# Kernel optimization log

Hardware: AMD Instinct MI355X
Metric: run time of the kernel (lower is better)

The kernel has to match this reference:

```python
import jax, jax.numpy as jnp
import numpy as np

B, L, D, H = 4, 1024, 1024, 16
HD = D // H


def setup_inputs() -> dict:
    key = jax.random.key(0)
    ks = jax.random.split(key, 64)
    it = iter(ks)

    def w(shape, s=0.02):
        return jax.random.normal(next(it), shape, dtype=jnp.float32) * s

    inp = {
        'seq_features': jax.random.normal(next(it), (B, L, D), dtype=jnp.float32),
        'struct_features': jax.random.normal(next(it), (B, L, D), dtype=jnp.float32),
        'attention_mask': jnp.ones((B, L), dtype=bool),
    }
    for p in ('s2s', 't2s'):
        inp[f'{p}_qw'] = w((D, D)); inp[f'{p}_qb'] = w((D,))
        inp[f'{p}_kw'] = w((D, D)); inp[f'{p}_kb'] = w((D,))
        inp[f'{p}_vw'] = w((D, D)); inp[f'{p}_vb'] = w((D,))
        inp[f'{p}_ow'] = w((D, D)); inp[f'{p}_ob'] = w((D,))
        inp[f'{p}_g'] = jnp.ones((D,), dtype=jnp.float32)
        inp[f'{p}_beta'] = jnp.zeros((D,), dtype=jnp.float32)
        inp[f'{p}_temp'] = jnp.ones((1,), dtype=jnp.float32)
    inp['fus_w1'] = w((2 * D, D)); inp['fus_b1'] = w((D,))
    inp['fus_w2'] = w((D, D)); inp['fus_b2'] = w((D,))
    return inp


def _layernorm(x, g, b, eps=1e-5):
    m = x.mean(-1, keepdims=True)
    v = ((x - m) ** 2).mean(-1, keepdims=True)
    return (x - m) / jnp.sqrt(v + eps) * g + b


def _cross_attn(q_in, kv_in, mask, qw, qb, kw, kb, vw, vb, ow, ob, g, beta, temp):
    # q_in, kv_in: (B, L, D); mask: (B, L) bool
    Q = (q_in @ qw + qb).reshape(B, L, H, HD).transpose(0, 2, 1, 3)
    K = (kv_in @ kw + kb).reshape(B, L, H, HD).transpose(0, 2, 1, 3)
    V = (kv_in @ vw + vb).reshape(B, L, H, HD).transpose(0, 2, 1, 3)
    scores = jnp.einsum('bhqd,bhkd->bhqk', Q, K) / np.float32(np.sqrt(HD))
    scores = scores / jnp.maximum(temp, 0.1)
    scores = jnp.where(mask[:, None, None, :], scores, -jnp.inf)
    aw = jax.nn.softmax(scores, axis=-1)  # dropout is identity in eval mode
    ctx = jnp.einsum('bhqk,bhkd->bhqd', aw, V).transpose(0, 2, 1, 3).reshape(B, L, D)
    out = _layernorm(ctx @ ow + ob + q_in, g, beta)
    return out, aw.mean(axis=1)


def _fusion(x, w1, b1, w2, b2):
    return jax.nn.gelu(x @ w1 + b1, approximate=False) @ w2 + b2


def reference(seq_features, struct_features, attention_mask,
              s2s_qw, s2s_qb, s2s_kw, s2s_kb, s2s_vw, s2s_vb, s2s_ow, s2s_ob, s2s_g, s2s_beta, s2s_temp,
              t2s_qw, t2s_qb, t2s_kw, t2s_kb, t2s_vw, t2s_vb, t2s_ow, t2s_ob, t2s_g, t2s_beta, t2s_temp,
              fus_w1, fus_b1, fus_w2, fus_b2):
    seq_upd, s2s_attn = _cross_attn(seq_features, struct_features, attention_mask,
                                    s2s_qw, s2s_qb, s2s_kw, s2s_kb, s2s_vw, s2s_vb,
                                    s2s_ow, s2s_ob, s2s_g, s2s_beta, s2s_temp)
    struct_upd, t2s_attn = _cross_attn(struct_features, seq_features, attention_mask,
                                       t2s_qw, t2s_qb, t2s_kw, t2s_kb, t2s_vw, t2s_vb,
                                       t2s_ow, t2s_ob, t2s_g, t2s_beta, t2s_temp)
    seq_fused = _fusion(jnp.concatenate([seq_upd, seq_features], axis=-1), fus_w1, fus_b1, fus_w2, fus_b2)
    struct_fused = _fusion(jnp.concatenate([struct_upd, struct_features], axis=-1), fus_w1, fus_b1, fus_w2, fus_b2)
    return seq_fused, struct_fused, s2s_attn, t2s_attn
```

## Files before the change

### kernel.cpp

```cpp
#include <hip/hip_runtime.h>
#include <hip/hip_bf16.h>
#include <stdint.h>
#include <stddef.h>

#define LL 1024
#define DD 1024

typedef __attribute__((ext_vector_type(8))) unsigned short ushort8;
typedef __attribute__((ext_vector_type(8))) __bf16 bf16x8;
typedef __attribute__((ext_vector_type(4))) __bf16 bf16x4;
typedef __attribute__((ext_vector_type(4))) float f32x4;
typedef __attribute__((ext_vector_type(4))) short short4v;
typedef unsigned short u16;

static __device__ __forceinline__ float b2f(u16 u) {
    union { uint32_t i; float f; } x; x.i = ((uint32_t)u) << 16; return x.f;
}
static __device__ __forceinline__ u16 f2b(float f) {
    union { float f; uint32_t i; } x; x.f = f;
    uint32_t r = (x.i + 0x7fffu + ((x.i >> 16) & 1u)) >> 16;
    return (u16)r;
}

#define GL16(gsrc, ldst)                                                      \
    __builtin_amdgcn_global_load_lds(                                         \
        (const __attribute__((address_space(1))) void*)(gsrc),                \
        (__attribute__((address_space(3))) void*)(ldst), 16, 0, 0)

struct WPtrs { const float* p[10]; };

__launch_bounds__(256)
__global__ void wcvt2_k(WPtrs wp, u16* __restrict__ dst)
{
    __shared__ float ls[64][65];
    const int bx = blockIdx.x;
    const float* src; size_t dbase; int n0, k0, Kd;
    if (bx < 2048) {
        const int mat = bx >> 8, t = bx & 255;
        n0 = (t >> 4) * 64; k0 = (t & 15) * 64;
        src = wp.p[mat]; dbase = (size_t)mat << 20; Kd = 1024;
    } else if (bx < 2560) {
        const int t = bx - 2048;
        n0 = (t >> 5) * 64; k0 = (t & 31) * 64;
        src = wp.p[8]; dbase = (size_t)8 << 20; Kd = 2048;
    } else {
        const int t = bx - 2560;
        n0 = (t >> 4) * 64; k0 = (t & 15) * 64;
        src = wp.p[9]; dbase = (size_t)10 << 20; Kd = 1024;
    }
    const int tid = threadIdx.x;
    const int rr = tid >> 2, cc0 = (tid & 3) * 16;
#pragma unroll
    for (int i = 0; i < 4; i++) {
        const f32x4 v = *(const f32x4*)(src + (size_t)(k0 + rr) * 1024 + n0 + cc0 + i * 4);
        *(f32x4*)&ls[rr][cc0 + i * 4] = v;
    }
    __syncthreads();
    const int nn = tid >> 2, ks0 = (tid & 3) * 16;
    u16* dp = dst + dbase + (size_t)(n0 + nn) * Kd + k0 + ks0;
#pragma unroll
    for (int i = 0; i < 4; i++) {
        short4v o;
#pragma unroll
        for (int j = 0; j < 4; j++) o[j] = (short)f2b(ls[ks0 + i * 4 + j][nn]);
        *(short4v*)(dp + i * 4) = o;
    }
}

__launch_bounds__(256)
__global__ void cvt_in_k(const float* __restrict__ a, const float* __restrict__ b,
                         u16* __restrict__ oa, u16* __restrict__ ob)
{
    const size_t i = ((size_t)blockIdx.x * 256 + threadIdx.x) * 8;
    f32x4 v0 = *(const f32x4*)(a + i), v1 = *(const f32x4*)(a + i + 4);
    f32x4 w0 = *(const f32x4*)(b + i), w1 = *(const f32x4*)(b + i + 4);
    ushort8 ra, rb;
#pragma unroll
    for (int j = 0; j < 4; j++) {
        ra[j] = f2b(v0[j]); ra[j + 4] = f2b(v1[j]);
        rb[j] = f2b(w0[j]); rb[j + 4] = f2b(w1[j]);
    }
    *(ushort8*)&oa[i] = ra;
    *(ushort8*)&ob[i] = rb;
}

__device__ __forceinline__ void gemm_core(
    const u16* __restrict__ A1, const u16* __restrict__ A2,
    const u16* __restrict__ WT, int K, int arow, int n0, int tid,
    u16* As, u16* Bt, f32x4 acc[4][4])
{
    const int lane = tid & 63, wid = tid >> 6;
    const int wr = wid >> 1, wc = wid & 1;
    const int fr = lane & 15, fq = lane >> 4;
    const int srow8 = lane >> 3, sslot = lane & 7;
    const int scol = ((sslot ^ srow8) * 8);
#pragma unroll
    for (int i = 0; i < 4; i++)
#pragma unroll
        for (int j = 0; j < 4; j++) acc[i][j] = f32x4{0.f, 0.f, 0.f, 0.f};

    auto stage = [&](int buf, int k0s) {
        const u16* Asrc = A1; int kc = k0s;
        if (A2 != nullptr && k0s >= 1024) { Asrc = A2; kc = k0s - 1024; }
#pragma unroll
        for (int p = 0; p < 4; p++) {
            const int row = p * 32 + wid * 8 + srow8;
            GL16(Asrc + (size_t)(arow + row) * 1024 + kc + scol,
                 As + buf * 8192 + (p * 32 + wid * 8) * 64);
            GL16(WT + (size_t)(n0 + row) * K + k0s + scol,
                 Bt + buf * 8192 + (p * 32 + wid * 8) * 64);
        }
    };

    stage(0, 0);
    __syncthreads();
    int cur = 0;
    for (int k0 = 0; k0 < K; k0 += 64) {
        if (k0 + 64 < K) stage(cur ^ 1, k0 + 64);
        const u16* Asb = As + cur * 8192;
        const u16* Btb = Bt + cur * 8192;
#pragma unroll
        for (int kk = 0; kk < 2; kk++) {
            const int rs = ((kk * 4 + fq) ^ (fr & 7)) * 8;
            bf16x8 af[4], bfv[4];
#pragma unroll
            for (int mi = 0; mi < 4; mi++)
                af[mi] = *(const bf16x8*)&Asb[(wr * 64 + mi * 16 + fr) * 64 + rs];
#pragma unroll
            for (int ni = 0; ni < 4; ni++)
                bfv[ni] = *(const bf16x8*)&Btb[(wc * 64 + ni * 16 + fr) * 64 + rs];
#pragma unroll
            for (int mi = 0; mi < 4; mi++)
#pragma unroll
                for (int ni = 0; ni < 4; ni++)
                    acc[mi][ni] = __builtin_amdgcn_mfma_f32_16x16x32_bf16(
                        af[mi], bfv[ni], acc[mi][ni], 0, 0, 0);
        }
        __syncthreads();
        cur ^= 1;
    }
}

struct ProjArgs {
    const u16* Au[2];
    const u16* wtQ[2]; const u16* wtK[2]; const u16* wtV[2];
    const float* bQ[2]; const float* bK[2]; const float* bV[2];
    const float* temp[2];
    u16* outQ[2]; u16* outK[2]; u16* outV[2];
};

__launch_bounds__(256)
__global__ void proj2_k(ProjArgs a)
{
    __shared__ __align__(16) u16 As[2 * 128 * 64];
    __shared__ __align__(16) u16 Bt[2 * 128 * 64];
    const int id = blockIdx.x;
    const int nid = (id & 7) * 192 + (id >> 3);
    const int pass = (nid >= 768);
    const int nid2 = nid - pass * 768;
    const int nt = nid2 % 24, mt = nid2 / 24;
    const int seg = nt >> 3, nc = (nt & 7) * 128, m0 = mt * 128;
    const u16* Au = a.Au[pass];
    const u16* WT = (seg == 0) ? a.wtQ[pass] : ((seg == 1) ? a.wtK[pass] : a.wtV[pass]);
    const float* bias = (seg == 0) ? a.bQ[pass] : ((seg == 1) ? a.bK[pass] : a.bV[pass]);
    u16* outQ = a.outQ[pass]; u16* outK = a.outK[pass]; u16* outV = a.outV[pass];
    const int tid = threadIdx.x, lane = tid & 63, wid = tid >> 6;
    const int wr = wid >> 1, wc = wid & 1, fr = lane & 15, fq = lane >> 4;
    const float qs = 1.44269504f * 0.125f / fmaxf(a.temp[pass][0], 0.1f);

    f32x4 acc[4][4];
    gemm_core(Au, nullptr, WT, 1024, m0, nc, tid, As, Bt, acc);

#pragma unroll
    for (int mi = 0; mi < 4; mi++) {
#pragma unroll
        for (int ni = 0; ni < 4; ni++) {
            const int col = nc + wc * 64 + ni * 16 + fr;
            const float bv = bias[col];
#pragma unroll
            for (int r = 0; r < 4; r++) {
                const int row = m0 + wr * 64 + mi * 16 + fq * 4 + r;
                const float v = acc[mi][ni][r] + bv;
                if (seg == 0) {
                    outQ[(size_t)row * 1024 + col] = f2b(v * qs);
                } else if (seg == 1) {
                    const int b2 = row >> 10, kk = row & 1023;
                    const int h2 = col >> 6, dd2 = col & 63;
                    const int kt = kk >> 4, fr2 = kk & 15;
                    const int plane = dd2 >> 5, fq2 = (dd2 >> 3) & 3, j = dd2 & 7;
                    outK[(size_t)(b2 * 16 + h2) * 65536 + kt * 1024 + plane * 512
                         + (fq2 * 16 + fr2) * 8 + j] = f2b(v);
                } else {
                    const int b2 = row >> 10, kk = row & 1023;
                    const int h2 = col >> 6, dd2 = col & 63;
                    outV[(size_t)(b2 * 16 + h2) * 65536 + (kk >> 4) * 1024
                         + (dd2 >> 4) * 256 + ((kk >> 2) & 3) * 64
                         + (dd2 & 15) * 4 + (kk & 3)] = f2b(v);
                }
            }
        }
    }
}

template <int EPI>
__launch_bounds__(256)
__global__ void mgemm_k(const u16* __restrict__ A1a, const u16* __restrict__ A1b,
                        const u16* __restrict__ A2a, const u16* __restrict__ A2b,
                        const u16* __restrict__ WTa, const u16* __restrict__ WTb,
                        const float* __restrict__ ba, const float* __restrict__ bb,
                        const float* __restrict__ ra, const float* __restrict__ rb,
                        void* __restrict__ oa_, void* __restrict__ ob_, int K)
{
    __shared__ __align__(16) u16 As[2 * 128 * 64];
    __shared__ __align__(16) u16 Bt[2 * 128 * 64];
    const int id = blockIdx.x;
    const int nid = (id & 7) * 64 + (id >> 3);
    const int n0 = (nid & 7) * 128, m0g = (nid >> 3) * 128;
    const int half = (m0g >= 4096), arow = m0g & 4095;
    const u16* A1 = half ? A1b : A1a;
    const u16* A2 = half ? A2b : A2a;
    const u16* WT = half ? WTb : WTa;
    const float* bias = half ? bb : ba;
    const float* res = half ? rb : ra;
    void* outp = half ? ob_ : oa_;
    const int tid = threadIdx.x, lane = tid & 63, wid = tid >> 6;
    const int wr = wid >> 1, wc = wid & 1, fr = lane & 15, fq = lane >> 4;

    f32x4 acc[4][4];
    gemm_core(A1, A2, WT, K, arow, n0, tid, As, Bt, acc);

#pragma unroll
    for (int mi = 0; mi < 4; mi++) {
#pragma unroll
        for (int ni = 0; ni < 4; ni++) {
            const int col = n0 + wc * 64 + ni * 16 + fr;
            const float bv = bias[col];
#pragma unroll
            for (int r = 0; r < 4; r++) {
                const int row = arow + wr * 64 + mi * 16 + fq * 4 + r;
                float v = acc[mi][ni][r] + bv;
                if (EPI == 1) {
                    v = 0.5f * v * (1.0f + erff(v * 0.70710678118f));
                    ((u16*)outp)[(size_t)row * 1024 + col] = f2b(v);
                } else if (EPI == 2) {
                    v += res[(size_t)row * 1024 + col];
                    ((float*)outp)[(size_t)row * 1024 + col] = v;
                } else {
                    ((float*)outp)[(size_t)row * 1024 + col] = v;
                }
            }
        }
    }
}

struct AttnArgs {
    const u16* Q[2]; const u16* KT[2]; const u16* Vt[2];
    u16* ctx[2]; float* iarr;
};

__global__ __launch_bounds__(512, 2)
void attnS3_k(AttnArgs a)
{
    const int id = blockIdx.x;
    const int b = id & 3, pass = (id >> 2) & 1, hg = (id >> 3) & 1;
    const int q0 = (id >> 4) * 64;
    const int tid = threadIdx.x, lane = tid & 63, wid = tid >> 6;
    const int fr = lane & 15, fq = lane >> 4;
    const int head = hg * 8 + wid;

    const u16* Q = a.Q[pass];
    bf16x8 bq0[4], bq1[4];
#pragma unroll
    for (int s = 0; s < 4; s++) {
        const u16* qp = Q + ((size_t)(b * LL + q0 + s * 16 + fr)) * DD + head * 64 + fq * 8;
        bq0[s] = *(const bf16x8*)(qp);
        bq1[s] = *(const bf16x8*)(qp + 32);
    }
    const u16* ktb = a.KT[pass] + (size_t)(b * 16 + head) * 65536 + lane * 8;
    const u16* vtb = a.Vt[pass] + (size_t)(b * 16 + head) * 65536 + lane * 4;

    float l[4] = {0.f, 0.f, 0.f, 0.f};
    f32x4 oa[4][4];
#pragma unroll
    for (int s = 0; s < 4; s++)
#pragma unroll
        for (int j = 0; j < 4; j++) oa[s][j] = f32x4{0.f, 0.f, 0.f, 0.f};

    for (int kt = 0; kt < 64; kt++) {
        const bf16x8 ka0 = *(const bf16x8*)(ktb + kt * 1024);
        const bf16x8 ka1 = *(const bf16x8*)(ktb + kt * 1024 + 512);
        short4v ps[4];
#pragma unroll
        for (int s = 0; s < 4; s++) {
            f32x4 c{0.f, 0.f, 0.f, 0.f};
            c = __builtin_amdgcn_mfma_f32_16x16x32_bf16(ka0, bq0[s], c, 0, 0, 0);
            c = __builtin_amdgcn_mfma_f32_16x16x32_bf16(ka1, bq1[s], c, 0, 0, 0);
            const float p0 = exp2f(c[0]), p1 = exp2f(c[1]);
            const float p2 = exp2f(c[2]), p3 = exp2f(c[3]);
            l[s] += (p0 + p1) + (p2 + p3);
            bf16x4 pb;
            pb[0] = (__bf16)p0; pb[1] = (__bf16)p1;
            pb[2] = (__bf16)p2; pb[3] = (__bf16)p3;
            ps[s] = __builtin_bit_cast(short4v, pb);
        }
        const u16* vp = vtb + (size_t)kt * 1024;
        const short4v va0 = *(const short4v*)(vp);
        const short4v va1 = *(const short4v*)(vp + 256);
        const short4v va2 = *(const short4v*)(vp + 512);
        const short4v va3 = *(const short4v*)(vp + 768);
#pragma unroll
        for (int s = 0; s < 4; s++) {
            oa[s][0] = __builtin_amdgcn_mfma_f32_16x16x16bf16_1k(va0, ps[s], oa[s][0], 0, 0, 0);
            oa[s][1] = __builtin_amdgcn_mfma_f32_16x16x16bf16_1k(va1, ps[s], oa[s][1], 0, 0, 0);
            oa[s][2] = __builtin_amdgcn_mfma_f32_16x16x16bf16_1k(va2, ps[s], oa[s][2], 0, 0, 0);
            oa[s][3] = __builtin_amdgcn_mfma_f32_16x16x16bf16_1k(va3, ps[s], oa[s][3], 0, 0, 0);
        }
    }
#pragma unroll
    for (int s = 0; s < 4; s++) {
        l[s] += __shfl_xor(l[s], 16);
        l[s] += __shfl_xor(l[s], 32);
        const float inv = 1.f / l[s];
        if (fq == 0) {
            const int qg = b * LL + q0 + s * 16 + fr;
            a.iarr[((pass * 16 + head) << 12) + qg] = inv;
        }
        u16* cp = a.ctx[pass] + ((size_t)(b * LL + q0 + s * 16 + fr)) * DD + head * 64 + fq * 4;
#pragma unroll
        for (int r = 0; r < 4; r++) {
            cp[r]      = f2b(oa[s][0][r] * inv);
            cp[16 + r] = f2b(oa[s][1][r] * inv);
            cp[32 + r] = f2b(oa[s][2][r] * inv);
            cp[48 + r] = f2b(oa[s][3][r] * inv);
        }
    }
}

__global__ __launch_bounds__(512, 2)
void meanM3_k(const u16* __restrict__ Q0, const u16* __restrict__ Q1,
              const u16* __restrict__ KT0, const u16* __restrict__ KT1,
              const float* __restrict__ iarr,
              float* __restrict__ d0, float* __restrict__ d1a,
              float* __restrict__ d1b)
{
    const int id = blockIdx.x;
    const int b = id & 3, pass = (id >> 2) & 1, kh = (id >> 3) & 1;
    const int q0 = (id >> 4) * 64;
    const int tid = threadIdx.x, lane = tid & 63, wid = tid >> 6;
    const int fr = lane & 15, fq = lane >> 4;
    const u16* Q = pass ? Q1 : Q0;
    const u16* KT = pass ? KT1 : KT0;
    __shared__ float il[16][64];
#pragma unroll
    for (int i = 0; i < 2; i++) {
        const int idx = tid + i * 512;
        const int h = idx >> 6, qq = idx & 63;
        il[h][qq] = iarr[((pass * 16 + h) << 12) + b * LL + q0 + qq];
    }
    __syncthreads();

    const int ktbase = kh * 32 + wid * 4;
    f32x4 msacc[4][4];
#pragma unroll
    for (int s = 0; s < 4; s++)
#pragma unroll
        for (int i = 0; i < 4; i++) msacc[s][i] = f32x4{0.f, 0.f, 0.f, 0.f};
    for (int h = 0; h < 16; h++) {
        bf16x8 cq0[4], cq1[4];
        float ih[4];
#pragma unroll
        for (int s = 0; s < 4; s++) {
            const u16* qp = Q + ((size_t)(b * LL + q0 + s * 16 + fr)) * DD + h * 64 + fq * 8;
            cq0[s] = *(const bf16x8*)(qp);
            cq1[s] = *(const bf16x8*)(qp + 32);
            ih[s] = il[h][s * 16 + fr];
        }
        const u16* kb = KT + (size_t)(b * 16 + h) * 65536 + lane * 8;
#pragma unroll
        for (int ktl = 0; ktl < 4; ktl++) {
            const int kt = ktbase + ktl;
            const bf16x8 ka0 = *(const bf16x8*)(kb + kt * 1024);
            const bf16x8 ka1 = *(const bf16x8*)(kb + kt * 1024 + 512);
#pragma unroll
            for (int s = 0; s < 4; s++) {
                f32x4 c{0.f, 0.f, 0.f, 0.f};
                c = __builtin_amdgcn_mfma_f32_16x16x32_bf16(ka0, cq0[s], c, 0, 0, 0);
                c = __builtin_amdgcn_mfma_f32_16x16x32_bf16(ka1, cq1[s], c, 0, 0, 0);
#pragma unroll
                for (int r = 0; r < 4; r++)
                    msacc[s][ktl][r] += exp2f(c[r]) * ih[s];
            }
        }
    }
#pragma unroll
    for (int s = 0; s < 4; s++) {
        float* dst; size_t rowbase;
        const int row = q0 + s * 16 + fr;
        if (pass == 0) {
            dst = d0; rowbase = (size_t)(b * LL + row) * 1024;
        } else {
            dst = (b < 2) ? d1a : d1b;
            rowbase = (size_t)((b & 1) * LL + row) * 1024;
        }
#pragma unroll
        for (int ktl = 0; ktl < 4; ktl++) {
            const f32x4 v = msacc[s][ktl] * (1.f / 16.f);
            *(f32x4*)&dst[rowbase + (ktbase + ktl) * 16 + fq * 4] = v;
        }
    }
}

__launch_bounds__(256)
__global__ void ln2_k(const float* __restrict__ y0, const float* __restrict__ y1,
                      const float* __restrict__ g0, const float* __restrict__ g1,
                      const float* __restrict__ be0, const float* __restrict__ be1,
                      u16* __restrict__ o0, u16* __restrict__ o1)
{
    const int rg = blockIdx.x, tid = threadIdx.x, lane = tid & 63, wid = tid >> 6;
    const int half = rg >> 12, rl = rg & 4095;
    const float* yp = (half ? y1 : y0) + (size_t)rl * 1024;
    const float* g = half ? g1 : g0;
    const float* be = half ? be1 : be0;
    u16* op = (half ? o1 : o0) + (size_t)rl * 1024;
    __shared__ float rsum[4], rsq[4];
    f32x4 v = *(const f32x4*)(yp + tid * 4);
    float s = v[0] + v[1] + v[2] + v[3];
    float sq = v[0]*v[0] + v[1]*v[1] + v[2]*v[2] + v[3]*v[3];
    for (int off = 1; off < 64; off <<= 1) {
        s  += __shfl_xor(s,  off, 64);
        sq += __shfl_xor(sq, off, 64);
    }
    if (lane == 0) { rsum[wid] = s; rsq[wid] = sq; }
    __syncthreads();
    const float S  = rsum[0] + rsum[1] + rsum[2] + rsum[3];
    const float SQ = rsq[0] + rsq[1] + rsq[2] + rsq[3];
    const float mean = S * (1.f / 1024.f);
    const float var  = SQ * (1.f / 1024.f) - mean * mean;
    const float rstd = rsqrtf(var + 1e-5f);
#pragma unroll
    for (int j = 0; j < 4; j++) {
        const int i = tid * 4 + j;
        op[i] = f2b((v[j] - mean) * rstd * g[i] + be[i]);
    }
}

extern "C" void kernel_launch(void* const* d_in, const int* in_sizes, int n_in,
                              void* d_out, int out_size, void* d_ws, size_t ws_size,
                              hipStream_t stream)
{
    (void)in_sizes; (void)n_in; (void)out_size; (void)ws_size;
    const float* seq = (const float*)d_in[0];
    const float* str = (const float*)d_in[1];
    const float* s2s_qb = (const float*)d_in[4];
    const float* s2s_kb = (const float*)d_in[6];
    const float* s2s_vb = (const float*)d_in[8];
    const float* s2s_ob = (const float*)d_in[10];
    const float* s2s_g  = (const float*)d_in[11];
    const float* s2s_be = (const float*)d_in[12];
    const float* s2s_t  = (const float*)d_in[13];
    const float* t2s_qb = (const float*)d_in[15];
    const float* t2s_kb = (const float*)d_in[17];
    const float* t2s_vb = (const float*)d_in[19];
    const float* t2s_ob = (const float*)d_in[21];
    const float* t2s_g  = (const float*)d_in[22];
    const float* t2s_be = (const float*)d_in[23];
    const float* t2s_t  = (const float*)d_in[24];
    const float* fb1 = (const float*)d_in[26];
    const float* fb2 = (const float*)d_in[28];

    char* ws = (char*)d_ws;
    u16*   Qs2s = (u16*)(ws);
    u16*   Ks2s = (u16*)(ws + ((size_t)8  << 20));
    u16*   Vs2s = (u16*)(ws + ((size_t)16 << 20));
    u16*   Qt2s = (u16*)(ws + ((size_t)24 << 20));
    u16*   Kt2s = (u16*)(ws + ((size_t)32 << 20));
    u16*   Vt2s = (u16*)(ws + ((size_t)40 << 20));
    float* mean1a = (float*)(ws + ((size_t)16 << 20));
    float* mean1b = (float*)(ws + ((size_t)40 << 20));
    float* y0   = (float*)(ws);
    float* y1   = (float*)(ws + ((size_t)24 << 20));
    u16*   sup  = (u16*)(ws + ((size_t)16 << 20));
    u16*   tup  = (u16*)(ws + ((size_t)40 << 20));
    u16*   sequ2 = (u16*)(ws);
    u16*   stru2 = (u16*)(ws + ((size_t)8 << 20));
    u16*   hid  = (u16*)(ws + ((size_t)24 << 20));
    u16*   fw2T = (u16*)(ws);

    float* out = (float*)d_out;
    const size_t M4 = (size_t)4 * 1024 * 1024;
    u16* wb = (u16*)d_out;
    u16* sequ = (u16*)((char*)d_out + ((size_t)32 << 20));
    u16* stru = (u16*)((char*)d_out + ((size_t)40 << 20));
    float* iarr = (float*)((char*)d_out + ((size_t)22 << 20));
    u16* ctx0 = (u16*)(out + 3 * M4);
    u16* ctx1 = ctx0 + (size_t)4096 * 1024;

    WPtrs wp;
    wp.p[0] = (const float*)d_in[3];
    wp.p[1] = (const float*)d_in[5];
    wp.p[2] = (const float*)d_in[7];
    wp.p[3] = (const float*)d_in[9];
    wp.p[4] = (const float*)d_in[14];
    wp.p[5] = (const float*)d_in[16];
    wp.p[6] = (const float*)d_in[18];
    wp.p[7] = (const float*)d_in[20];
    wp.p[8] = (const float*)d_in[25];
    wp.p[9] = (const float*)d_in[27];
    wcvt2_k<<<2816, 256, 0, stream>>>(wp, wb);
    cvt_in_k<<<2048, 256, 0, stream>>>(seq, str, sequ, stru);

    const dim3 gb(256);

    ProjArgs pa;
    pa.Au[0] = sequ;                         pa.Au[1] = stru;
    pa.wtQ[0] = wb;                          pa.wtQ[1] = wb + ((size_t)4 << 20);
    pa.wtK[0] = wb + ((size_t)5 << 20);      pa.wtK[1] = wb + ((size_t)1 << 20);
    pa.wtV[0] = wb + ((size_t)6 << 20);      pa.wtV[1] = wb + ((size_t)2 << 20);
    pa.bQ[0] = s2s_qb;  pa.bQ[1] = t2s_qb;
    pa.bK[0] = t2s_kb;  pa.bK[1] = s2s_kb;
    pa.bV[0] = t2s_vb;  pa.bV[1] = s2s_vb;
    pa.temp[0] = s2s_t; pa.temp[1] = t2s_t;
    pa.outQ[0] = Qs2s;  pa.outQ[1] = Qt2s;
    pa.outK[0] = Kt2s;  pa.outK[1] = Ks2s;
    pa.outV[0] = Vt2s;  pa.outV[1] = Vs2s;
    proj2_k<<<1536, gb, 0, stream>>>(pa);

    AttnArgs aa;
    aa.Q[0] = Qs2s;  aa.Q[1] = Qt2s;
    aa.KT[0] = Ks2s; aa.KT[1] = Kt2s;
    aa.Vt[0] = Vs2s; aa.Vt[1] = Vt2s;
    aa.ctx[0] = ctx0; aa.ctx[1] = ctx1;
    aa.iarr = iarr;
    attnS3_k<<<256, 512, 0, stream>>>(aa);

    meanM3_k<<<256, 512, 0, stream>>>(Qs2s, Qt2s, Ks2s, Kt2s, iarr,
                                      out + 2 * M4, mean1a, mean1b);

    mgemm_k<2><<<512, gb, 0, stream>>>(
        ctx0, ctx1, nullptr, nullptr,
        wb + ((size_t)3 << 20), wb + ((size_t)7 << 20),
        s2s_ob, t2s_ob, seq, str, y0, y1, 1024);

    hipMemcpyAsync(out + 3 * M4, mean1a, (size_t)8 << 20,
                   hipMemcpyDeviceToDevice, stream);
    hipMemcpyAsync((char*)(out + 3 * M4) + ((size_t)8 << 20), mean1b,
                   (size_t)8 << 20, hipMemcpyDeviceToDevice, stream);

    ln2_k<<<8192, gb, 0, stream>>>(y0, y1, s2s_g, t2s_g, s2s_be, t2s_be, sup, tup);

    cvt_in_k<<<2048, 256, 0, stream>>>(seq, str, sequ2, stru2);

    mgemm_k<1><<<512, gb, 0, stream>>>(
        sup, tup, sequ2, stru2,
        wb + ((size_t)8 << 20), wb + ((size_t)8 << 20),
        fb1, fb1, nullptr, nullptr, hid, hid + (size_t)4096 * 1024, 2048);

    hipMemcpyAsync(fw2T, wb + ((size_t)10 << 20), (size_t)2 << 20,
                   hipMemcpyDeviceToDevice, stream);

    mgemm_k<3><<<512, gb, 0, stream>>>(
        hid, hid + (size_t)4096 * 1024, nullptr, nullptr,
        fw2T, fw2T, fb2, fb2, nullptr, nullptr, out, out + M4, 1024);
}
```

Before: 345.1 us.

## Fuse conversion kernels, store pre-LN residual in bf16, drop mean-attention copies

The input bf16 conversion is merged into the weight-transpose kernel, and the second input conversion is folded into the layernorm kernel, which removes two launches. The out-projection epilogue now writes the residual sum as bf16 instead of fp32, halving that intermediate's traffic. The mean-attention kernel is reordered after the out-projection GEMM and writes directly into the output buffer, which removes two 8 MB device-to-device copies. The workspace is re-laid out to allow this, at the cost of an extra bf16 rounding of the pre-layernorm values.

Result: faster. 333.2 us (median of 2 runs) (-3.4%).

```diff
diff --git a/kernel.cpp b/kernel.cpp
--- a/kernel.cpp
+++ b/kernel.cpp
@@ -7,6 +7,7 @@
 #define DD 1024
 
 typedef __attribute__((ext_vector_type(8))) unsigned short ushort8;
+typedef __attribute__((ext_vector_type(4))) unsigned short ushort4v;
 typedef __attribute__((ext_vector_type(8))) __bf16 bf16x8;
 typedef __attribute__((ext_vector_type(4))) __bf16 bf16x4;
 typedef __attribute__((ext_vector_type(4))) float f32x4;
@@ -30,10 +31,27 @@
 struct WPtrs { const float* p[10]; };
 
 __launch_bounds__(256)
-__global__ void wcvt2_k(WPtrs wp, u16* __restrict__ dst)
+__global__ void wcvt3_k(WPtrs wp, u16* __restrict__ dst,
+                        const float* __restrict__ ia, const float* __restrict__ ib,
+                        u16* __restrict__ oa, u16* __restrict__ ob)
 {
     __shared__ float ls[64][65];
     const int bx = blockIdx.x;
+    const int tid = threadIdx.x;
+    if (bx >= 2816) {
+        const size_t i = ((size_t)(bx - 2816) * 256 + tid) * 8;
+        f32x4 v0 = *(const f32x4*)(ia + i), v1 = *(const f32x4*)(ia + i + 4);
+        f32x4 w0 = *(const f32x4*)(ib + i), w1 = *(const f32x4*)(ib + i + 4);
+        ushort8 ra, rb;
+#pragma unroll
+        for (int j = 0; j < 4; j++) {
+            ra[j] = f2b(v0[j]); ra[j + 4] = f2b(v1[j]);
+            rb[j] = f2b(w0[j]); rb[j + 4] = f2b(w1[j]);
+        }
+        *(ushort8*)&oa[i] = ra;
+        *(ushort8*)&ob[i] = rb;
+        return;
+    }
     const float* src; size_t dbase; int n0, k0, Kd;
     if (bx < 2048) {
         const int mat = bx >> 8, t = bx & 255;
@@ -48,7 +66,6 @@
         n0 = (t >> 4) * 64; k0 = (t & 15) * 64;
         src = wp.p[9]; dbase = (size_t)10 << 20; Kd = 1024;
     }
-    const int tid = threadIdx.x;
     const int rr = tid >> 2, cc0 = (tid & 3) * 16;
 #pragma unroll
     for (int i = 0; i < 4; i++) {
@@ -65,23 +82,6 @@
         for (int j = 0; j < 4; j++) o[j] = (short)f2b(ls[ks0 + i * 4 + j][nn]);
         *(short4v*)(dp + i * 4) = o;
     }
-}
-
-__launch_bounds__(256)
-__global__ void cvt_in_k(const float* __restrict__ a, const float* __restrict__ b,
-                         u16* __restrict__ oa, u16* __restrict__ ob)
-{
-    const size_t i = ((size_t)blockIdx.x * 256 + threadIdx.x) * 8;
-    f32x4 v0 = *(const f32x4*)(a + i), v1 = *(const f32x4*)(a + i + 4);
-    f32x4 w0 = *(const f32x4*)(b + i), w1 = *(const f32x4*)(b + i + 4);
-    ushort8 ra, rb;
-#pragma unroll
-    for (int j = 0; j < 4; j++) {
-        ra[j] = f2b(v0[j]); ra[j + 4] = f2b(v1[j]);
-        rb[j] = f2b(w0[j]); rb[j + 4] = f2b(w1[j]);
-    }
-    *(ushort8*)&oa[i] = ra;
-    *(ushort8*)&ob[i] = rb;
 }
 
 __device__ __forceinline__ void gemm_core(
@@ -242,9 +242,9 @@
                 if (EPI == 1) {
                     v = 0.5f * v * (1.0f + erff(v * 0.70710678118f));
                     ((u16*)outp)[(size_t)row * 1024 + col] = f2b(v);
-                } else if (EPI == 2) {
+                } else if (EPI == 4) {
                     v += res[(size_t)row * 1024 + col];
-                    ((float*)outp)[(size_t)row * 1024 + col] = v;
+                    ((u16*)outp)[(size_t)row * 1024 + col] = f2b(v);
                 } else {
                     ((float*)outp)[(size_t)row * 1024 + col] = v;
                 }
@@ -340,8 +340,7 @@
 void meanM3_k(const u16* __restrict__ Q0, const u16* __restrict__ Q1,
               const u16* __restrict__ KT0, const u16* __restrict__ KT1,
               const float* __restrict__ iarr,
-              float* __restrict__ d0, float* __restrict__ d1a,
-              float* __restrict__ d1b)
+              float* __restrict__ d0, float* __restrict__ d1)
 {
     const int id = blockIdx.x;
     const int b = id & 3, pass = (id >> 2) & 1, kh = (id >> 3) & 1;
@@ -392,16 +391,10 @@
             }
         }
     }
+    float* dst = pass ? d1 : d0;
 #pragma unroll
     for (int s = 0; s < 4; s++) {
-        float* dst; size_t rowbase;
-        const int row = q0 + s * 16 + fr;
-        if (pass == 0) {
-            dst = d0; rowbase = (size_t)(b * LL + row) * 1024;
-        } else {
-            dst = (b < 2) ? d1a : d1b;
-            rowbase = (size_t)((b & 1) * LL + row) * 1024;
-        }
+        const size_t rowbase = (size_t)(b * LL + q0 + s * 16 + fr) * 1024;
 #pragma unroll
         for (int ktl = 0; ktl < 4; ktl++) {
             const f32x4 v = msacc[s][ktl] * (1.f / 16.f);
@@ -411,19 +404,39 @@
 }
 
 __launch_bounds__(256)
-__global__ void ln2_k(const float* __restrict__ y0, const float* __restrict__ y1,
-                      const float* __restrict__ g0, const float* __restrict__ g1,
-                      const float* __restrict__ be0, const float* __restrict__ be1,
-                      u16* __restrict__ o0, u16* __restrict__ o1)
-{
-    const int rg = blockIdx.x, tid = threadIdx.x, lane = tid & 63, wid = tid >> 6;
+__global__ void lncvt_k(const u16* __restrict__ y0, const u16* __restrict__ y1,
+                        const float* __restrict__ g0, const float* __restrict__ g1,
+                        const float* __restrict__ be0, const float* __restrict__ be1,
+                        u16* __restrict__ o0, u16* __restrict__ o1,
+                        const float* __restrict__ ia, const float* __restrict__ ib,
+                        u16* __restrict__ oa, u16* __restrict__ ob)
+{
+    const int rg = blockIdx.x, tid = threadIdx.x;
+    if (rg >= 8192) {
+        const size_t i = ((size_t)(rg - 8192) * 256 + tid) * 8;
+        f32x4 v0 = *(const f32x4*)(ia + i), v1 = *(const f32x4*)(ia + i + 4);
+        f32x4 w0 = *(const f32x4*)(ib + i), w1 = *(const f32x4*)(ib + i + 4);
+        ushort8 ra, rb;
+#pragma unroll
+        for (int j = 0; j < 4; j++) {
+            ra[j] = f2b(v0[j]); ra[j + 4] = f2b(v1[j]);
+            rb[j] = f2b(w0[j]); rb[j + 4] = f2b(w1[j]);
+        }
+        *(ushort8*)&oa[i] = ra;
+        *(ushort8*)&ob[i] = rb;
+        return;
+    }
+    const int lane = tid & 63, wid = tid >> 6;
     const int half = rg >> 12, rl = rg & 4095;
-    const float* yp = (half ? y1 : y0) + (size_t)rl * 1024;
+    const u16* yp = (half ? y1 : y0) + (size_t)rl * 1024;
     const float* g = half ? g1 : g0;
     const float* be = half ? be1 : be0;
     u16* op = (half ? o1 : o0) + (size_t)rl * 1024;
     __shared__ float rsum[4], rsq[4];
-    f32x4 v = *(const f32x4*)(yp + tid * 4);
+    const ushort4v u = *(const ushort4v*)(yp + tid * 4);
+    float v[4];
+#pragma unroll
+    for (int j = 0; j < 4; j++) v[j] = b2f(u[j]);
     float s = v[0] + v[1] + v[2] + v[3];
     float sq = v[0]*v[0] + v[1]*v[1] + v[2]*v[2] + v[3]*v[3];
     for (int off = 1; off < 64; off <<= 1) {
@@ -475,16 +488,15 @@
     u16*   Qt2s = (u16*)(ws + ((size_t)24 << 20));
     u16*   Kt2s = (u16*)(ws + ((size_t)32 << 20));
     u16*   Vt2s = (u16*)(ws + ((size_t)40 << 20));
-    float* mean1a = (float*)(ws + ((size_t)16 << 20));
-    float* mean1b = (float*)(ws + ((size_t)40 << 20));
-    float* y0   = (float*)(ws);
-    float* y1   = (float*)(ws + ((size_t)24 << 20));
-    u16*   sup  = (u16*)(ws + ((size_t)16 << 20));
-    u16*   tup  = (u16*)(ws + ((size_t)40 << 20));
-    u16*   sequ2 = (u16*)(ws);
-    u16*   stru2 = (u16*)(ws + ((size_t)8 << 20));
-    u16*   hid  = (u16*)(ws + ((size_t)24 << 20));
-    u16*   fw2T = (u16*)(ws);
+    u16*   ya   = (u16*)(ws + ((size_t)16 << 20));
+    u16*   yb   = (u16*)(ws + ((size_t)40 << 20));
+    u16*   sup  = (u16*)(ws);
+    u16*   tup  = (u16*)(ws + ((size_t)24 << 20));
+    u16*   sequ2 = (u16*)(ws + ((size_t)8 << 20));
+    u16*   stru2 = (u16*)(ws + ((size_t)32 << 20));
+    u16*   hidA = (u16*)(ws + ((size_t)16 << 20));
+    u16*   hidB = (u16*)(ws + ((size_t)40 << 20));
+    u16*   fw2T = (u16*)(ws + ((size_t)8 << 20));
 
     float* out = (float*)d_out;
     const size_t M4 = (size_t)4 * 1024 * 1024;
@@ -506,8 +518,7 @@
     wp.p[7] = (const float*)d_in[20];
     wp.p[8] = (const float*)d_in[25];
     wp.p[9] = (const float*)d_in[27];
-    wcvt2_k<<<2816, 256, 0, stream>>>(wp, wb);
-    cvt_in_k<<<2048, 256, 0, stream>>>(seq, str, sequ, stru);
+    wcvt3_k<<<4864, 256, 0, stream>>>(wp, wb, seq, str, sequ, stru);
 
     const dim3 gb(256);
 
@@ -533,32 +544,26 @@
     aa.iarr = iarr;
     attnS3_k<<<256, 512, 0, stream>>>(aa);
 
-    meanM3_k<<<256, 512, 0, stream>>>(Qs2s, Qt2s, Ks2s, Kt2s, iarr,
-                                      out + 2 * M4, mean1a, mean1b);
-
-    mgemm_k<2><<<512, gb, 0, stream>>>(
+    mgemm_k<4><<<512, gb, 0, stream>>>(
         ctx0, ctx1, nullptr, nullptr,
         wb + ((size_t)3 << 20), wb + ((size_t)7 << 20),
-        s2s_ob, t2s_ob, seq, str, y0, y1, 1024);
-
-    hipMemcpyAsync(out + 3 * M4, mean1a, (size_t)8 << 20,
-                   hipMemcpyDeviceToDevice, stream);
-    hipMemcpyAsync((char*)(out + 3 * M4) + ((size_t)8 << 20), mean1b,
-                   (size_t)8 << 20, hipMemcpyDeviceToDevice, stream);
-
-    ln2_k<<<8192, gb, 0, stream>>>(y0, y1, s2s_g, t2s_g, s2s_be, t2s_be, sup, tup);
-
-    cvt_in_k<<<2048, 256, 0, stream>>>(seq, str, sequ2, stru2);
+        s2s_ob, t2s_ob, seq, str, ya, yb, 1024);
+
+    meanM3_k<<<256, 512, 0, stream>>>(Qs2s, Qt2s, Ks2s, Kt2s, iarr,
+                                      out + 2 * M4, out + 3 * M4);
+
+    lncvt_k<<<10240, gb, 0, stream>>>(ya, yb, s2s_g, t2s_g, s2s_be, t2s_be,
+                                      sup, tup, seq, str, sequ2, stru2);
 
     mgemm_k<1><<<512, gb, 0, stream>>>(
         sup, tup, sequ2, stru2,
         wb + ((size_t)8 << 20), wb + ((size_t)8 << 20),
-        fb1, fb1, nullptr, nullptr, hid, hid + (size_t)4096 * 1024, 2048);
+        fb1, fb1, nullptr, nullptr, hidA, hidB, 2048);
 
     hipMemcpyAsync(fw2T, wb + ((size_t)10 << 20), (size_t)2 << 20,
                    hipMemcpyDeviceToDevice, stream);
 
     mgemm_k<3><<<512, gb, 0, stream>>>(
-        hid, hid + (size_t)4096 * 1024, nullptr, nullptr,
+        hidA, hidB, nullptr, nullptr,
         fw2T, fw2T, fb2, fb2, nullptr, nullptr, out, out + M4, 1024);
 }
```
